# Optimization experiments

Hardware: AMD Instinct MI355X
Metric: run time of the kernel (lower is better)

Reference implementation:

```python
import jax, jax.numpy as jnp
import numpy as np
from functools import partial


def advect(f, vx, vy):
    """Semi-Lagrangian advection with bilinear interpolation and periodic wrap.
    Faithful to the torch version, including its xy-indexed meshgrid."""
    rows, cols = f.shape
    # torch.meshgrid(arange(rows), arange(cols), indexing='xy') == np.meshgrid semantics
    cell_ys, cell_xs = jnp.meshgrid(jnp.arange(rows), jnp.arange(cols), indexing='xy')
    center_xs = (cell_xs - vx).ravel()
    center_ys = (cell_ys - vy).ravel()
    left_ix = jnp.floor(center_xs).astype(jnp.int32)
    top_ix = jnp.floor(center_ys).astype(jnp.int32)
    rw = center_xs - left_ix  # right weight
    bw = center_ys - top_ix   # bottom weight
    left_ix = jnp.mod(left_ix, rows)
    right_ix = jnp.mod(left_ix + 1, rows)
    top_ix = jnp.mod(top_ix, cols)
    bot_ix = jnp.mod(top_ix + 1, cols)
    flat_f = ((1 - rw) * ((1 - bw) * f[left_ix, top_ix] + bw * f[left_ix, bot_ix])
              + rw * ((1 - bw) * f[right_ix, top_ix] + bw * f[right_ix, bot_ix]))
    return flat_f.reshape(rows, cols)


def project(vx, vy):
    """Approximate pressure projection: 10 Jacobi iterations of a 5-point stencil."""
    h = 1.0 / vx.shape[0]
    div = -0.5 * h * (jnp.roll(vx, -1, axis=0) - jnp.roll(vx, 1, axis=0)
                      + jnp.roll(vy, -1, axis=1) - jnp.roll(vy, 1, axis=1))

    def jacobi(k, p):
        return (div + jnp.roll(p, 1, axis=0) + jnp.roll(p, -1, axis=0)
                + jnp.roll(p, 1, axis=1) + jnp.roll(p, -1, axis=1)) / 4.0

    p = jax.lax.fori_loop(0, 10, jacobi, jnp.zeros_like(vx))
    vx = vx - 0.5 * (jnp.roll(p, -1, axis=0) - jnp.roll(p, 1, axis=0)) / h
    vy = vy - 0.5 * (jnp.roll(p, -1, axis=1) - jnp.roll(p, 1, axis=1)) / h
    return vx, vy


def simulate(vx, vy, smoke, num_time_steps):
    def step(carry, _):
        vx, vy, smoke = carry
        vx_upd = advect(vx, vx, vy)
        vy_upd = advect(vy, vx, vy)
        vx, vy = project(vx_upd, vy_upd)
        smoke = advect(smoke, vx, vy)
        return (vx, vy, smoke), None

    (vx, vy, smoke), _ = jax.lax.scan(step, (vx, vy, smoke), None, length=num_time_steps)
    return smoke


def setup_inputs() -> dict:
    key = jax.random.key(0)
    k1, k2, k3 = jax.random.split(key, 3)
    N = 2048
    smoke = jax.random.uniform(k1, (N, N), dtype=jnp.float32)
    init_vx = jax.random.normal(k2, (N, N), dtype=jnp.float32)
    init_vy = jax.random.normal(k3, (N, N), dtype=jnp.float32)
    return {"smoke": smoke, "init_vx": init_vx, "init_vy": init_vy,
            "num_time_steps": 20}


def reference(smoke, init_vx, init_vy, num_time_steps):
    return simulate(init_vx, init_vy, smoke, num_time_steps)
```

## Files before the change

kernel.cpp:

```cpp
#include <hip/hip_runtime.h>

namespace {

constexpr int N = 2048;
constexpr int MASK = N - 1;
constexpr int SH = 11;
constexpr float H = 1.0f / (float)N;

using f32x2 = __attribute__((ext_vector_type(2))) float;


__device__ __forceinline__ float dpp_left(float x) {
  return __int_as_float(__builtin_amdgcn_update_dpp(
      0, __float_as_int(x), 0x111 , 0xF, 0xF, true));
}
__device__ __forceinline__ float dpp_right(float x) {
  return __int_as_float(__builtin_amdgcn_update_dpp(
      0, __float_as_int(x), 0x101 , 0xF, 0xF, true));
}

__global__ __launch_bounds__(256) void advect_vel_k(
    const float* __restrict__ vx, const float* __restrict__ vy,
    float* __restrict__ ovx, float* __restrict__ ovy) {
  int bid = blockIdx.x;
  int sb = ((bid & 7) << 11) | (bid >> 3);
  int idx = sb * 256 + threadIdx.x;
  int i = idx >> SH, j = idx & MASK;
  float cx = (float)i - vx[idx];
  float cy = (float)j - vy[idx];
  float fx = floorf(cx), fy = floorf(cy);
  float rw = cx - fx, bw = cy - fy;
  int l = ((int)fx) & MASK;
  int t = ((int)fy) & MASK;
  int r = (l + 1) & MASK;
  int b = (t + 1) & MASK;
  int i00 = (l << SH) | t, i01 = (l << SH) | b;
  int i10 = (r << SH) | t, i11 = (r << SH) | b;
  float omr = 1.0f - rw, omb = 1.0f - bw;
  float w00 = omr * omb, w01 = omr * bw, w10 = rw * omb, w11 = rw * bw;
  ovx[idx] = w00 * vx[i00] + w01 * vx[i01] + w10 * vx[i10] + w11 * vx[i11];
  ovy[idx] = w00 * vy[i00] + w01 * vy[i01] + w10 * vy[i10] + w11 * vy[i11];
}

__device__ __forceinline__ float4 jac_row(float4 dd, float4 vu, float4 vd, float4 o) {
  float pl = dpp_left(o.w);
  float pr = dpp_right(o.x);
  f32x2 dlo = {dd.x, dd.y}, dhi = {dd.z, dd.w};
  f32x2 vulo = {vu.x, vu.y}, vuhi = {vu.z, vu.w};
  f32x2 vdlo = {vd.x, vd.y}, vdhi = {vd.z, vd.w};
  f32x2 lft = {pl, o.x};
  f32x2 mid = {o.y, o.z};
  f32x2 rgt = {o.w, pr};
  f32x2 lo = (dlo + vulo + vdlo + lft + mid) * 0.25f;
  f32x2 hi = (dhi + vuhi + vdhi + mid + rgt) * 0.25f;
  return float4{lo.x, lo.y, hi.x, hi.y};
}

__device__ __forceinline__ void div_p1(float4 au, float4 ad, float4 b,
                                       float4& dq, float4& pq) {
  float yl = dpp_left(b.w);
  float yr = dpp_right(b.x);
  constexpr float s = -0.5f * H;
  f32x2 vlo = f32x2{ad.x, ad.y} - f32x2{au.x, au.y};
  f32x2 vhi = f32x2{ad.z, ad.w} - f32x2{au.z, au.w};
  f32x2 hlo = f32x2{b.y, b.z} - f32x2{yl, b.x};
  f32x2 hhi = f32x2{b.w, yr} - f32x2{b.y, b.z};
  f32x2 dlo = (vlo + hlo) * s;
  f32x2 dhi = (vhi + hhi) * s;
  f32x2 plo = dlo * 0.25f;
  f32x2 phi = dhi * 0.25f;
  dq = float4{dlo.x, dlo.y, dhi.x, dhi.y};
  pq = float4{plo.x, plo.y, phi.x, phi.y};
}

__global__ __launch_bounds__(512, 6) void project_smoke_k(
    const float* __restrict__ vx, const float* __restrict__ vy,
    const float* __restrict__ f,
    float* __restrict__ ovx, float* __restrict__ ovy,
    float* __restrict__ of) {
  __shared__ __align__(16) float pA[90 * 64];
  __shared__ __align__(16) float pB[90 * 64];

  const int tid = threadIdx.x;
  const int bid = blockIdx.x;
  const int sbid = ((bid & 7) << 8) | (bid >> 3);
  const int tile_i = sbid >> 6;
  const int tile_j = sbid & 63;
  const int bi = tile_i * 64 - 11;
  const int cj0 = tile_j * 32 - 16;

  for (int e = tid; e < 86 * 16; e += 512) {
    int row = e >> 4;
    int u = e & 15;
    int gi = (bi + row) & MASK;
    int gj = (cj0 + u * 4) & MASK;
    int gg = (gi << SH) | gj;
    *(float4*)&pA[(row + 1) * 64 + u * 4] = *(const float4*)&vx[gg];
    *(float4*)&pB[(row + 1) * 64 + u * 4] = *(const float4*)&vy[gg];
  }
  __syncthreads();

  const int g = tid >> 4;
  const int c0 = (tid & 15) * 4;
  const bool act = (g < 29);
  const int r0 = 3 * g;
  float4 p[3], d[3];
#pragma unroll
  for (int q = 0; q < 3; ++q) { p[q] = float4{0,0,0,0}; d[q] = float4{0,0,0,0}; }

  if (act) {
    const int lb = r0 * 64 + c0;
    float4 a0 = *(const float4*)&pA[lb];
    float4 a1 = *(const float4*)&pA[lb + 64];
    float4 a2 = *(const float4*)&pA[lb + 128];
    float4 a3 = *(const float4*)&pA[lb + 192];
    float4 a4 = *(const float4*)&pA[lb + 256];
    float4 b0 = *(const float4*)&pB[lb + 64];
    float4 b1 = *(const float4*)&pB[lb + 128];
    float4 b2 = *(const float4*)&pB[lb + 192];
    div_p1(a0, a2, b0, d[0], p[0]);
    div_p1(a1, a3, b1, d[1], p[1]);
    div_p1(a2, a4, b2, d[2], p[2]);
  }
  __syncthreads();

#pragma unroll
  for (int k = 0; k < 9; ++k) {
    float* w = (k & 1) ? pB : pA;
    if (act) {
      *(float4*)&w[(r0 + 1) * 64 + c0] = p[0];
      *(float4*)&w[(r0 + 3) * 64 + c0] = p[2];
    }
    __syncthreads();
    if (act) {
      float4 up = *(const float4*)&w[(r0 + 0) * 64 + c0];
      float4 dn = *(const float4*)&w[(r0 + 4) * 64 + c0];
      float4 o0 = p[0], o1 = p[1];
      p[0] = jac_row(d[0], up, o1, o0);
      p[1] = jac_row(d[1], o0, p[2], o1);
      p[2] = jac_row(d[2], o1, dn, p[2]);
    }
  }

  if (act) {
    *(float4*)&pB[(r0 + 1) * 64 + c0] = p[0];
    *(float4*)&pB[(r0 + 2) * 64 + c0] = p[1];
    *(float4*)&pB[(r0 + 3) * 64 + c0] = p[2];
  }
  __syncthreads();

  const float c = 0.5f / H;
#pragma unroll
  for (int q = 0; q < 4; ++q) {
    int pth = tid + q * 512;
    int oi = pth >> 5, oj = pth & 31;
    int gi = tile_i * 64 + oi;
    int gj = tile_j * 32 + oj;
    int gg = (gi << SH) | gj;
    float vxc = vx[gg];
    float vyc = vy[gg];
    float nvx = vxc - c * (pB[(13 + oi) * 64 + 16 + oj] - pB[(11 + oi) * 64 + 16 + oj]);
    float nvy = vyc - c * (pB[(12 + oi) * 64 + 17 + oj] - pB[(12 + oi) * 64 + 15 + oj]);
    ovx[gg] = nvx;
    ovy[gg] = nvy;
    float cx = (float)gi - nvx;
    float cy = (float)gj - nvy;
    float fx = floorf(cx), fy = floorf(cy);
    float rw = cx - fx, bw = cy - fy;
    int l = ((int)fx) & MASK;
    int t = ((int)fy) & MASK;
    int r = (l + 1) & MASK;
    int b = (t + 1) & MASK;
    float f00 = f[(l << SH) | t];
    float f01 = f[(l << SH) | b];
    float f10 = f[(r << SH) | t];
    float f11 = f[(r << SH) | b];
    float omr = 1.0f - rw, omb = 1.0f - bw;
    of[gg] = omr * (omb * f00 + bw * f01) + rw * (omb * f10 + bw * f11);
  }
}

}

extern "C" void kernel_launch(void* const* d_in, const int* in_sizes, int n_in,
                              void* d_out, int out_size, void* d_ws, size_t ws_size,
                              hipStream_t stream) {
  const float* smoke_in = (const float*)d_in[0];
  const float* vx_in    = (const float*)d_in[1];
  const float* vy_in    = (const float*)d_in[2];
  float* out = (float*)d_out;

  const size_t fsz = (size_t)N * N;
  float* base = (float*)d_ws;
  float* A  = base + 0 * fsz;
  float* B  = base + 1 * fsz;
  float* C  = base + 2 * fsz;
  float* D  = base + 3 * fsz;
  float* SA = base + 4 * fsz;

  dim3 ablk(256), agrd((N * N) / 256);
  dim3 pblk(512), pgrd(32 * 64);
  const int steps = 20;

  const float* ssrc = smoke_in;

  advect_vel_k<<<agrd, ablk, 0, stream>>>(vx_in, vy_in, C, D);

  for (int t = 0; t < steps; ++t) {
    float* sdst = (t & 1) ? out : SA;
    project_smoke_k<<<pgrd, pblk, 0, stream>>>(C, D, ssrc, A, B, sdst);
    ssrc = sdst;
    if (t < steps - 1)
      advect_vel_k<<<agrd, ablk, 0, stream>>>(A, B, C, D);
  }
}
```

Baseline: 1.117 ms.

## Move smoke advection from projection epilogue into fused velocity-and-smoke advect kernel

Smoke advection is taken out of the projection kernel's epilogue and combined with the next step's velocity advection in one kernel that reuses the bilinear indices and weights for smoke, vx and vy. The last step uses a smoke-only advect kernel. This is meant to lighten the projection kernel and share the interpolation setup and the gather locality across three fields. In exchange, the advect kernel becomes heavier and gather-bound, and the projection's freshly computed velocities are no longer used in registers.

```diff
diff --git a/kernel.cpp b/kernel.cpp
--- a/kernel.cpp
+++ b/kernel.cpp
@@ -42,6 +42,55 @@
   ovy[idx] = w00 * vy[i00] + w01 * vy[i01] + w10 * vy[i10] + w11 * vy[i11];
 }
 
+__global__ __launch_bounds__(256) void advect_all_k(
+    const float* __restrict__ f,
+    const float* __restrict__ vx, const float* __restrict__ vy,
+    float* __restrict__ of, float* __restrict__ ovx, float* __restrict__ ovy) {
+  int bid = blockIdx.x;
+  int sb = ((bid & 7) << 11) | (bid >> 3);
+  int idx = sb * 256 + threadIdx.x;
+  int i = idx >> SH, j = idx & MASK;
+  float cx = (float)i - vx[idx];
+  float cy = (float)j - vy[idx];
+  float fx = floorf(cx), fy = floorf(cy);
+  float rw = cx - fx, bw = cy - fy;
+  int l = ((int)fx) & MASK;
+  int t = ((int)fy) & MASK;
+  int r = (l + 1) & MASK;
+  int b = (t + 1) & MASK;
+  int i00 = (l << SH) | t, i01 = (l << SH) | b;
+  int i10 = (r << SH) | t, i11 = (r << SH) | b;
+  float omr = 1.0f - rw, omb = 1.0f - bw;
+  float w00 = omr * omb, w01 = omr * bw, w10 = rw * omb, w11 = rw * bw;
+  of[idx]  = w00 * f[i00]  + w01 * f[i01]  + w10 * f[i10]  + w11 * f[i11];
+  ovx[idx] = w00 * vx[i00] + w01 * vx[i01] + w10 * vx[i10] + w11 * vx[i11];
+  ovy[idx] = w00 * vy[i00] + w01 * vy[i01] + w10 * vy[i10] + w11 * vy[i11];
+}
+
+__global__ __launch_bounds__(256) void advect_smoke_k(
+    const float* __restrict__ f,
+    const float* __restrict__ vx, const float* __restrict__ vy,
+    float* __restrict__ of) {
+  int bid = blockIdx.x;
+  int sb = ((bid & 7) << 11) | (bid >> 3);
+  int idx = sb * 256 + threadIdx.x;
+  int i = idx >> SH, j = idx & MASK;
+  float cx = (float)i - vx[idx];
+  float cy = (float)j - vy[idx];
+  float fx = floorf(cx), fy = floorf(cy);
+  float rw = cx - fx, bw = cy - fy;
+  int l = ((int)fx) & MASK;
+  int t = ((int)fy) & MASK;
+  int r = (l + 1) & MASK;
+  int b = (t + 1) & MASK;
+  float f00 = f[(l << SH) | t];
+  float f01 = f[(l << SH) | b];
+  float f10 = f[(r << SH) | t];
+  float f11 = f[(r << SH) | b];
+  float omr = 1.0f - rw, omb = 1.0f - bw;
+  of[idx] = omr * (omb * f00 + bw * f01) + rw * (omb * f10 + bw * f11);
+}
+
 __device__ __forceinline__ float4 jac_row(float4 dd, float4 vu, float4 vd, float4 o) {
   float pl = dpp_left(o.w);
   float pr = dpp_right(o.x);
@@ -73,11 +122,9 @@
   pq = float4{plo.x, plo.y, phi.x, phi.y};
 }
 
-__global__ __launch_bounds__(512, 6) void project_smoke_k(
-    const float* __restrict__ vx, const float* __restrict__ vy,
-    const float* __restrict__ f,
-    float* __restrict__ ovx, float* __restrict__ ovy,
-    float* __restrict__ of) {
+__global__ __launch_bounds__(512, 6) void project_k(
+    const float* __restrict__ vx, const float* __restrict__ vy,
+    float* __restrict__ ovx, float* __restrict__ ovy) {
   __shared__ __align__(16) float pA[90 * 64];
   __shared__ __align__(16) float pB[90 * 64];
 
@@ -163,20 +210,6 @@
     float nvy = vyc - c * (pB[(12 + oi) * 64 + 17 + oj] - pB[(12 + oi) * 64 + 15 + oj]);
     ovx[gg] = nvx;
     ovy[gg] = nvy;
-    float cx = (float)gi - nvx;
-    float cy = (float)gj - nvy;
-    float fx = floorf(cx), fy = floorf(cy);
-    float rw = cx - fx, bw = cy - fy;
-    int l = ((int)fx) & MASK;
-    int t = ((int)fy) & MASK;
-    int r = (l + 1) & MASK;
-    int b = (t + 1) & MASK;
-    float f00 = f[(l << SH) | t];
-    float f01 = f[(l << SH) | b];
-    float f10 = f[(r << SH) | t];
-    float f11 = f[(r << SH) | b];
-    float omr = 1.0f - rw, omb = 1.0f - bw;
-    of[gg] = omr * (omb * f00 + bw * f01) + rw * (omb * f10 + bw * f11);
   }
 }
 
@@ -207,10 +240,13 @@
   advect_vel_k<<<agrd, ablk, 0, stream>>>(vx_in, vy_in, C, D);
 
   for (int t = 0; t < steps; ++t) {
+    project_k<<<pgrd, pblk, 0, stream>>>(C, D, A, B);
     float* sdst = (t & 1) ? out : SA;
-    project_smoke_k<<<pgrd, pblk, 0, stream>>>(C, D, ssrc, A, B, sdst);
+    if (t < steps - 1) {
+      advect_all_k<<<agrd, ablk, 0, stream>>>(ssrc, A, B, sdst, C, D);
+    } else {
+      advect_smoke_k<<<agrd, ablk, 0, stream>>>(ssrc, A, B, sdst);
+    }
     ssrc = sdst;
-    if (t < steps - 1)
-      advect_vel_k<<<agrd, ablk, 0, stream>>>(A, B, C, D);
-  }
-}
+  }
+}
```

New measurement: 1.149 ms. 2.9% more time.
